# Kernel optimization log

Hardware: AMD Instinct MI355X
Metric: run time of the kernel (lower is better)

The kernel has to match this reference:

```python
import jax, jax.numpy as jnp
import numpy as np

# Quantization constants (match init_kwargs)
A_SCALE = 0.05   # activation scale
W_SCALE = 0.01   # weight scale
A_QN, A_QP = -128, 127  # int8 activation clamp range
STRIDE = (2, 2)
PADDING = ((1, 1), (1, 1))
DILATION = (1, 1)


def setup_inputs() -> dict:
    key = jax.random.key(0)
    kx, kw = jax.random.split(key)
    # Input activations [N, C_in, H, W]
    x = jax.random.normal(kx, (32, 256, 56, 56), dtype=jnp.float32)
    # Int4 weights in [-8, 7], stored as int-valued float32 (unpacked form of weight_packed)
    w = jax.random.randint(kw, (256, 256, 3, 3), -8, 8).astype(jnp.float32)
    return {"x": x, "w": w}


def reference(x, w):
    # Activation int8 quantization: round-half-to-even (matches torch.round), clamp to [a_qn, a_qp]
    x_q = jnp.clip(jnp.round(x / A_SCALE), A_QN, A_QP)
    # Int4xInt8 GEMM over unfolded patches == conv on quantized integer values.
    # Values are small ints so fp32 accumulation is exact (|acc| <= 2304*127*8 < 2^24).
    acc = jax.lax.conv_general_dilated(
        x_q, w,
        window_strides=STRIDE,
        padding=PADDING,
        rhs_dilation=DILATION,
        dimension_numbers=("NCHW", "OIHW", "NCHW"),
    )  # [N, C_out, H_out, W_out] = [32, 256, 28, 28]
    # Dequantize: acc_int32 * (a_scale * w_scale); bias=False; out_dtype=float32
    y = acc * (A_SCALE * W_SCALE)
    return y.astype(jnp.float32)
```

## Files before the change

### kernel.cpp

```cpp
#include <hip/hip_runtime.h>
#include <stdint.h>

typedef int v4i __attribute__((ext_vector_type(4)));

#define N_IMG 32
#define C_IN 256
#define H_IN 56
#define W_IN 56
#define C_OUT 256
#define H_OUT 28
#define W_OUT 28
#define H_PAD 58
#define W_PAD 58
#define SP_TOT (N_IMG*H_OUT*W_OUT)

#define XPAD_BYTES ((size_t)N_IMG*H_PAD*W_PAD*C_IN)
#define WQ_BYTES   ((size_t)9*C_OUT*C_IN)

__device__ __forceinline__ void glds16(const int8_t* g, int8_t* l) {
    __builtin_amdgcn_global_load_lds(
        (const __attribute__((address_space(1))) void*)g,
        (__attribute__((address_space(3))) void*)l, 16, 0, 0);
}

__global__ __launch_bounds__(256) void quant_kernel(const float* __restrict__ x,
                                                    int8_t* __restrict__ xpad) {
    __shared__ uint32_t ldsu[W_IN * 65];
    const int n = blockIdx.x, hp = blockIdx.y;
    const int t = threadIdx.x;
    int8_t* row = xpad + ((size_t)n * H_PAD + hp) * W_PAD * C_IN;

    if (hp == 0 || hp == H_PAD - 1) {
        #pragma unroll
        for (int i = 0; i < 4; ++i) {
            int idx = i * 256 + t;
            if (idx < 928) *(int4*)(row + idx * 16) = (int4){0, 0, 0, 0};
        }
        return;
    }
    const int h = hp - 1;
    const float* xp = x + (size_t)n * C_IN * H_IN * W_IN + (size_t)h * W_IN;

    #pragma unroll
    for (int it = 0; it < 14; ++it) {
        int idx = it * 256 + t;
        int c4 = idx / 56, w = idx - c4 * 56;
        const float* p = xp + (size_t)(c4 * 4) * (H_IN * W_IN) + w;
        uint32_t u = 0;
        #pragma unroll
        for (int i = 0; i < 4; ++i) {
            float qv = rintf(p[(size_t)i * (H_IN * W_IN)] / 0.05f);
            qv = fminf(fmaxf(qv, -128.0f), 127.0f);
            u |= ((uint32_t)((int)qv & 255)) << (8 * i);
        }
        ldsu[w * 65 + c4] = u;
    }
    if (t < 32) {
        int8_t* p = (t < 16) ? (row + t * 16)
                             : (row + (size_t)(W_PAD - 1) * C_IN + (t - 16) * 16);
        *(int4*)p = (int4){0, 0, 0, 0};
    }
    __syncthreads();

    int8_t* op = row + C_IN;
    #pragma unroll
    for (int it = 0; it < 14; ++it) {
        int idx = it * 256 + t;
        int w = idx >> 6, c4 = idx & 63;
        *(uint32_t*)(op + (size_t)w * C_IN + c4 * 4) = ldsu[w * 65 + c4];
    }
}

__global__ __launch_bounds__(256) void wq_kernel(const float* __restrict__ w,
                                                 int8_t* __restrict__ wq) {
    int idx = blockIdx.x * 256 + threadIdx.x;
    int ci  = idx & 255;
    int co  = (idx >> 8) & 255;
    int khw = idx >> 16;
    float v = w[(size_t)(co * C_IN + ci) * 9 + khw];
    wq[idx] = (int8_t)(int)rintf(v);
}

__global__ __launch_bounds__(256) void conv_kernel(const int8_t* __restrict__ xpad,
                                                   const int8_t* __restrict__ wq,
                                                   float* __restrict__ out) {
    __shared__ __align__(16) int8_t lds[49152];
    const int t = threadIdx.x;
    const int wave = t >> 6, lane = t & 63;
    const int q = lane >> 4, s = lane & 15;
    const int co_blk = blockIdx.y * 128;
    const int sp_blk = blockIdx.x * 64;

    const int row_l4 = wave * 4 + q;
    const int chunk  = (lane & 15) ^ row_l4;
    const int8_t* gw = wq + (size_t)(co_blk + row_l4) * 256 + chunk * 16;

    const int8_t* ga[4];
    #pragma unroll
    for (int r = 0; r < 4; ++r) {
        int sp = sp_blk + r * 16 + row_l4;
        int n  = sp / (H_OUT * W_OUT);
        int rm = sp - n * (H_OUT * W_OUT);
        int ho = rm / W_OUT;
        int wo = rm - ho * W_OUT;
        ga[r] = xpad + ((size_t)(n * H_PAD + ho * 2) * W_PAD + wo * 2) * C_IN + chunk * 16;
    }

    int8_t* lw = lds + wave * 1024;
    int8_t* la = lds + 32768 + wave * 1024;

    const int cw = (wave >> 1) * 64;
    const int sw = (wave & 1) * 32;
    int out_base[2];
    #pragma unroll
    for (int j = 0; j < 2; ++j) {
        int sp = sp_blk + sw + j * 16 + s;
        int n  = sp / (H_OUT * W_OUT);
        int rm = sp - n * (H_OUT * W_OUT);
        int ho = rm / W_OUT;
        int wo = rm - ho * W_OUT;
        out_base[j] = n * (C_OUT * H_OUT * W_OUT) + ho * W_OUT + wo;
    }

    v4i acc[4][2];
    #pragma unroll
    for (int i = 0; i < 4; ++i)
        #pragma unroll
        for (int j = 0; j < 2; ++j)
            acc[i][j] = (v4i){0, 0, 0, 0};

    for (int kh = 0; kh < 3; ++kh) {
        for (int kwv = 0; kwv < 3; ++kwv) {
            __syncthreads();
            const int woff = (kh * 3 + kwv) * (C_OUT * C_IN);
            const int aoff = (kh * W_PAD + kwv) * C_IN;
            #pragma unroll
            for (int r = 0; r < 8; ++r)
                glds16(gw + woff + r * 4096, lw + r * 4096);
            #pragma unroll
            for (int r = 0; r < 4; ++r)
                glds16(ga[r] + aoff, la + r * 4096);
            __syncthreads();

            #pragma unroll
            for (int ks = 0; ks < 4; ++ks) {
                const int st = ((ks * 4 + q) ^ s) * 16;
                v4i a[4], b[2];
                #pragma unroll
                for (int i = 0; i < 4; ++i)
                    a[i] = *(const v4i*)(lds + (cw + i * 16 + s) * 256 + st);
                #pragma unroll
                for (int j = 0; j < 2; ++j)
                    b[j] = *(const v4i*)(lds + 32768 + (sw + j * 16 + s) * 256 + st);
                #pragma unroll
                for (int i = 0; i < 4; ++i)
                    #pragma unroll
                    for (int j = 0; j < 2; ++j)
                        acc[i][j] = __builtin_amdgcn_mfma_i32_16x16x64_i8(
                            a[i], b[j], acc[i][j], 0, 0, 0);
            }
        }
    }

    #pragma unroll
    for (int j = 0; j < 2; ++j) {
        #pragma unroll
        for (int i = 0; i < 4; ++i) {
            const int co0 = co_blk + cw + i * 16 + q * 4;
            #pragma unroll
            for (int r = 0; r < 4; ++r) {
                out[(size_t)out_base[j] + (size_t)(co0 + r) * (H_OUT * W_OUT)] =
                    (float)acc[i][j][r] * 0.0005f;
            }
        }
    }
}

extern "C" void kernel_launch(void* const* d_in, const int* in_sizes, int n_in,
                              void* d_out, int out_size, void* d_ws, size_t ws_size,
                              hipStream_t stream) {
    const float* x = (const float*)d_in[0];
    const float* w = (const float*)d_in[1];
    float* out = (float*)d_out;
    int8_t* xpad = (int8_t*)d_ws;
    int8_t* wqb  = xpad + XPAD_BYTES;

    quant_kernel<<<dim3(N_IMG, H_PAD), 256, 0, stream>>>(x, xpad);
    wq_kernel<<<(9 * C_OUT * C_IN) / 256, 256, 0, stream>>>(w, wqb);
    conv_kernel<<<dim3(SP_TOT / 64, 2), 256, 0, stream>>>(xpad, wqb, out);
}
```

Before: 217.8 us.

## Vectorize quant loads with shuffle transpose and shrink conv output tile

The quant kernel now reads float4 along width and uses two cross-lane shuffles to transpose bytes, so each lane packs four channels. Channels are permuted consistently (c4 + 64*j), and the weight quant kernel reorders ci to match. The conv kernel's tile drops from 128 to 64 output channels per block and LDS from 48KB to 32KB. That doubles the grid and raises occupancy, at the cost of loading activation tiles twice as often.

```diff
diff --git a/kernel.cpp b/kernel.cpp
--- a/kernel.cpp
+++ b/kernel.cpp
@@ -15,7 +15,7 @@
 #define SP_TOT (N_IMG*H_OUT*W_OUT)
 
 #define XPAD_BYTES ((size_t)N_IMG*H_PAD*W_PAD*C_IN)
-#define WQ_BYTES   ((size_t)9*C_OUT*C_IN)
+
 
 __device__ __forceinline__ void glds16(const int8_t* g, int8_t* l) {
     __builtin_amdgcn_global_load_lds(
@@ -41,19 +41,29 @@
     const int h = hp - 1;
     const float* xp = x + (size_t)n * C_IN * H_IN * W_IN + (size_t)h * W_IN;
 
+    const int wv = t >> 6, lane = t & 63;
+    const int j = lane >> 4, w4 = lane & 15;
+    const int w4c = (w4 < 14) ? w4 : 13;
+
     #pragma unroll
-    for (int it = 0; it < 14; ++it) {
-        int idx = it * 256 + t;
-        int c4 = idx / 56, w = idx - c4 * 56;
-        const float* p = xp + (size_t)(c4 * 4) * (H_IN * W_IN) + w;
+    for (int it = 0; it < 16; ++it) {
+        const int c4 = it * 4 + wv;
+        const float4 v = *(const float4*)(xp + (size_t)(c4 + 64 * j) * (H_IN * W_IN) + w4c * 4);
+        float f[4] = {v.x, v.y, v.z, v.w};
         uint32_t u = 0;
         #pragma unroll
         for (int i = 0; i < 4; ++i) {
-            float qv = rintf(p[(size_t)i * (H_IN * W_IN)] / 0.05f);
+            float qv = rintf(f[i] / 0.05f);
             qv = fminf(fmaxf(qv, -128.0f), 127.0f);
             u |= ((uint32_t)((int)qv & 255)) << (8 * i);
         }
-        ldsu[w * 65 + c4] = u;
+        uint32_t p1 = __shfl_xor(u, 16);
+        uint32_t tt = (j & 1) ? (((p1 >> 8) & 0x00FF00FFu) | (u & 0xFF00FF00u))
+                              : ((u & 0x00FF00FFu) | ((p1 << 8) & 0xFF00FF00u));
+        uint32_t p2 = __shfl_xor(tt, 32);
+        uint32_t rr = (j & 2) ? ((p2 >> 16) | (tt & 0xFFFF0000u))
+                              : ((tt & 0x0000FFFFu) | (p2 << 16));
+        if (w4 < 14) ldsu[(w4 * 4 + j) * 65 + c4] = rr;
     }
     if (t < 32) {
         int8_t* p = (t < 16) ? (row + t * 16)
@@ -74,9 +84,10 @@
 __global__ __launch_bounds__(256) void wq_kernel(const float* __restrict__ w,
                                                  int8_t* __restrict__ wq) {
     int idx = blockIdx.x * 256 + threadIdx.x;
-    int ci  = idx & 255;
+    int p   = idx & 255;
     int co  = (idx >> 8) & 255;
     int khw = idx >> 16;
+    int ci  = 64 * (p & 3) + (p >> 2);
     float v = w[(size_t)(co * C_IN + ci) * 9 + khw];
     wq[idx] = (int8_t)(int)rintf(v);
 }
@@ -84,21 +95,21 @@
 __global__ __launch_bounds__(256) void conv_kernel(const int8_t* __restrict__ xpad,
                                                    const int8_t* __restrict__ wq,
                                                    float* __restrict__ out) {
-    __shared__ __align__(16) int8_t lds[49152];
+    __shared__ __align__(16) int8_t lds[32768];
     const int t = threadIdx.x;
     const int wave = t >> 6, lane = t & 63;
     const int q = lane >> 4, s = lane & 15;
-    const int co_blk = blockIdx.y * 128;
+    const int co_blk = blockIdx.y * 64;
     const int sp_blk = blockIdx.x * 64;
 
-    const int row_l4 = wave * 4 + q;
-    const int chunk  = (lane & 15) ^ row_l4;
-    const int8_t* gw = wq + (size_t)(co_blk + row_l4) * 256 + chunk * 16;
+    const int rl   = t >> 4;
+    const int chunk = (t & 15) ^ (rl & 15);
+    const int8_t* gw = wq + (size_t)(co_blk + rl) * 256 + chunk * 16;
 
     const int8_t* ga[4];
     #pragma unroll
     for (int r = 0; r < 4; ++r) {
-        int sp = sp_blk + r * 16 + row_l4;
+        int sp = sp_blk + r * 16 + rl;
         int n  = sp / (H_OUT * W_OUT);
         int rm = sp - n * (H_OUT * W_OUT);
         int ho = rm / W_OUT;
@@ -106,10 +117,7 @@
         ga[r] = xpad + ((size_t)(n * H_PAD + ho * 2) * W_PAD + wo * 2) * C_IN + chunk * 16;
     }
 
-    int8_t* lw = lds + wave * 1024;
-    int8_t* la = lds + 32768 + wave * 1024;
-
-    const int cw = (wave >> 1) * 64;
+    const int cw = (wave >> 1) * 32;
     const int sw = (wave & 1) * 32;
     int out_base[2];
     #pragma unroll
@@ -122,9 +130,9 @@
         out_base[j] = n * (C_OUT * H_OUT * W_OUT) + ho * W_OUT + wo;
     }
 
-    v4i acc[4][2];
+    v4i acc[2][2];
     #pragma unroll
-    for (int i = 0; i < 4; ++i)
+    for (int i = 0; i < 2; ++i)
         #pragma unroll
         for (int j = 0; j < 2; ++j)
             acc[i][j] = (v4i){0, 0, 0, 0};
@@ -135,25 +143,25 @@
             const int woff = (kh * 3 + kwv) * (C_OUT * C_IN);
             const int aoff = (kh * W_PAD + kwv) * C_IN;
             #pragma unroll
-            for (int r = 0; r < 8; ++r)
-                glds16(gw + woff + r * 4096, lw + r * 4096);
+            for (int r = 0; r < 4; ++r)
+                glds16(gw + woff + r * 4096, lds + r * 4096 + t * 16);
             #pragma unroll
             for (int r = 0; r < 4; ++r)
-                glds16(ga[r] + aoff, la + r * 4096);
+                glds16(ga[r] + aoff, lds + 16384 + r * 4096 + t * 16);
             __syncthreads();
 
             #pragma unroll
             for (int ks = 0; ks < 4; ++ks) {
                 const int st = ((ks * 4 + q) ^ s) * 16;
-                v4i a[4], b[2];
+                v4i a[2], b[2];
                 #pragma unroll
-                for (int i = 0; i < 4; ++i)
+                for (int i = 0; i < 2; ++i)
                     a[i] = *(const v4i*)(lds + (cw + i * 16 + s) * 256 + st);
                 #pragma unroll
                 for (int j = 0; j < 2; ++j)
-                    b[j] = *(const v4i*)(lds + 32768 + (sw + j * 16 + s) * 256 + st);
+                    b[j] = *(const v4i*)(lds + 16384 + (sw + j * 16 + s) * 256 + st);
                 #pragma unroll
-                for (int i = 0; i < 4; ++i)
+                for (int i = 0; i < 2; ++i)
                     #pragma unroll
                     for (int j = 0; j < 2; ++j)
                         acc[i][j] = __builtin_amdgcn_mfma_i32_16x16x64_i8(
@@ -165,7 +173,7 @@
     #pragma unroll
     for (int j = 0; j < 2; ++j) {
         #pragma unroll
-        for (int i = 0; i < 4; ++i) {
+        for (int i = 0; i < 2; ++i) {
             const int co0 = co_blk + cw + i * 16 + q * 4;
             #pragma unroll
             for (int r = 0; r < 4; ++r) {
@@ -187,5 +195,5 @@
 
     quant_kernel<<<dim3(N_IMG, H_PAD), 256, 0, stream>>>(x, xpad);
     wq_kernel<<<(9 * C_OUT * C_IN) / 256, 256, 0, stream>>>(w, wqb);
-    conv_kernel<<<dim3(SP_TOT / 64, 2), 256, 0, stream>>>(xpad, wqb, out);
+    conv_kernel<<<dim3(SP_TOT / 64, C_OUT / 64), 256, 0, stream>>>(xpad, wqb, out);
 }
```

Measured after the change: 191.9 us. 11.9% less time.
